# Kernel optimization log

Measured on AMD Instinct MI355X. Metric: run time of the kernel, lower is better.

## Reference

```python
import jax, jax.numpy as jnp
import numpy as np

N_MODES = 64


def setup_inputs() -> dict:
    key = jax.random.key(0)
    k1, k2, k3 = jax.random.split(key, 3)
    B, Cin, S = 32, 128, 8192
    H, Hc, M = 4, 32, N_MODES  # n_heads, head_channels, n_modes (Cout = H*Hc = 128)
    x = jax.random.normal(k1, (B, Cin, S), dtype=jnp.float32)
    # per-head init scale: std = 0.01 * 2**h (matches _init_weights)
    scale = (0.01 * 2.0 ** jnp.arange(H, dtype=jnp.float32)).reshape(H, 1, 1, 1)
    w_real = jax.random.normal(k2, (H, Cin, Hc, M), dtype=jnp.float32) * scale
    w_imag = jax.random.normal(k3, (H, Cin, Hc, M), dtype=jnp.float32) * scale
    return {"x": x, "w_real": w_real, "w_imag": w_imag}


def reference(x, w_real, w_imag):
    B, Cin, S = x.shape
    H, _, Hc, M = w_real.shape
    Cout = H * Hc
    x_ft = jnp.fft.rfft(x, axis=-1)                 # [B, Cin, F] complex64
    F = x_ft.shape[-1]
    M = min(M, F)                                    # static
    w = (w_real + 1j * w_imag).astype(x_ft.dtype)    # [H, Cin, Hc, M]
    # fused batched complex contraction over all heads/modes at once
    out = jnp.einsum('bim,hiom->bhom', x_ft[:, :, :M], w[..., :M])  # [B, H, Hc, M]
    out = out.reshape(B, Cout, M)                    # head h -> channels [h*Hc, (h+1)*Hc)
    out_ft = jnp.zeros((B, Cout, F), dtype=x_ft.dtype).at[:, :, :M].set(out)
    return jnp.fft.irfft(out_ft, n=S, axis=-1)       # [B, Cout, S] float32
```

## Files before the change

kernel.cpp:

```cpp
#include <hip/hip_runtime.h>
#include <cstdio>

#define S_LEN 8192
#define NM 64

typedef short s8v __attribute__((ext_vector_type(8)));
typedef float f4  __attribute__((ext_vector_type(4)));
typedef _Float16 h8 __attribute__((ext_vector_type(8)));

static __device__ inline unsigned short f2bf(float f) {
    unsigned int u = __builtin_bit_cast(unsigned int, f);
    u = (u + 0x7FFFu + ((u >> 16) & 1u)) >> 16;
    return (unsigned short)u;
}
static __device__ inline float bf2f(unsigned short h) {
    unsigned int u = ((unsigned int)h) << 16;
    return __builtin_bit_cast(float, u);
}

#define SW32(r, k) (((r) * 32) + ((k) ^ ((((r) >> 1) & 3) << 3)))

static __device__ __forceinline__ void glds16(const void* g, void* l) {
    __builtin_amdgcn_global_load_lds(
        (const __attribute__((address_space(1))) unsigned int*)g,
        (__attribute__((address_space(3))) unsigned int*)l, 16, 0, 0);
}

__global__ __launch_bounds__(256) void gen_master(float* __restrict__ tab) {
    int p = blockIdx.x * 256 + threadIdx.x;
    tab[p] = cosf((float)p * (6.28318530717958647692f / (float)S_LEN));
}

__global__ __launch_bounds__(256) void gen_tables(const float* __restrict__ tab,
                                                  short* __restrict__ T1fH,
                                                  short* __restrict__ T1fL,
                                                  _Float16* __restrict__ Bimg) {
    int tid = blockIdx.x * 256 + threadIdx.x;
    {
        int tile = tid >> 12;
        int sb = tile >> 2, kc = tile & 3;
        int uw = tid & 4095;
        int c = uw >> 5, rest = uw & 31;
        int k = kc * 32 + rest;
        int s = sb * 128 + c;
        int m = k >> 1;
        int p = (m * s + ((k & 1) << 11)) & (S_LEN - 1);
        float v = tab[p];
        unsigned short h = f2bf(v);
        T1fH[tid] = (short)h;
        T1fL[tid] = (short)f2bf(v - bf2f(h));
    }
    {
        int tk = tid >> 13;
        int us = tid & 8191;
        int c = us >> 6;
        int wl = us & 63;
        int slot = wl >> 3, e = wl & 7;
        int k = ((slot ^ (c & 7)) << 3) | e;
        int kg = tk * 64 + k;
        int m = c >> 1;
        int p = (m * kg + ((c & 1) << 11)) & (S_LEN - 1);
        Bimg[tid] = (_Float16)tab[p];
    }
}

__global__ __launch_bounds__(512, 4) void dft_fwd_mfma(const float* __restrict__ x,
        const _Float16* __restrict__ Bimg, float* __restrict__ P) {
    __shared__ _Float16 abh[2][4096], abl[2][4096];
    __shared__ _Float16 bb[2][8192];
    const int t = threadIdx.x;
    const int lane = t & 63, w = t >> 6;
    const int rl = lane & 15, kq = lane >> 4;
    const int wr = w >> 2, wc = w & 3;
    const int row0 = blockIdx.x * 64;
    const int ks = blockIdx.y;
    const int rA = t >> 3, sA = t & 7;
    const size_t xrow = (size_t)(row0 + rA) * S_LEN + (size_t)ks * 1024 + (size_t)sA * 8;
    const int usA = rA * 64 + ((sA ^ (rA & 7)) << 3);
    const size_t bby = (size_t)ks * 16 * 16384 + (size_t)t * 32;

    f4 acc[2][2];
    #pragma unroll
    for (int i = 0; i < 2; ++i)
        #pragma unroll
        for (int j = 0; j < 2; ++j) acc[i][j] = (f4){0.f, 0.f, 0.f, 0.f};

    f4 aP[3][2];
    h8 bP[2][2];

    #define LA_(SC, A0, A1) { A0 = *(const f4*)&x[xrow + (size_t)(SC) * 64];       \
                              A1 = *(const f4*)&x[xrow + (size_t)(SC) * 64 + 4]; }
    #define LB_(SC, B0, B1) { const char* g = (const char*)Bimg + bby +            \
                                  (size_t)(SC) * 16384;                            \
                              B0 = *(const h8*)g; B1 = *(const h8*)(g + 16); }
    #define CV_(A0, A1, NXT) { h8 hv, lv;                                          \
        _Pragma("unroll")                                                          \
        for (int e = 0; e < 4; ++e) {                                              \
            float f = A0[e]; _Float16 hh = (_Float16)f;                            \
            hv[e] = hh; lv[e] = (_Float16)(f - (float)hh);                         \
        }                                                                          \
        _Pragma("unroll")                                                          \
        for (int e = 0; e < 4; ++e) {                                              \
            float f = A1[e]; _Float16 hh = (_Float16)f;                            \
            hv[4 + e] = hh; lv[4 + e] = (_Float16)(f - (float)hh);                 \
        }                                                                          \
        *(h8*)&abh[NXT][usA] = hv;                                                 \
        *(h8*)&abl[NXT][usA] = lv; }
    #define WB_(B0, B1, NXT) { *(h8*)&bb[NXT][t * 16] = B0;                        \
                               *(h8*)&bb[NXT][t * 16 + 8] = B1; }
    #define MM_(CUR) { _Pragma("unroll")                                           \
        for (int ksl = 0; ksl < 2; ++ksl) {                                        \
            const int sb_ = ksl * 4 + kq;                                          \
            h8 Ah0, Al0, Ah1, Al1, Bv0, Bv1;                                       \
            { int r = wr * 32 + rl;      int u = r * 64 + ((sb_ ^ (r & 7)) << 3);  \
              Ah0 = *(const h8*)&abh[CUR][u]; Al0 = *(const h8*)&abl[CUR][u]; }    \
            { int r = wr * 32 + 16 + rl; int u = r * 64 + ((sb_ ^ (r & 7)) << 3);  \
              Ah1 = *(const h8*)&abh[CUR][u]; Al1 = *(const h8*)&abl[CUR][u]; }    \
            { int c = wc * 32 + rl;      int u = c * 64 + ((sb_ ^ (c & 7)) << 3);  \
              Bv0 = *(const h8*)&bb[CUR][u]; }                                     \
            { int c = wc * 32 + 16 + rl; int u = c * 64 + ((sb_ ^ (c & 7)) << 3);  \
              Bv1 = *(const h8*)&bb[CUR][u]; }                                     \
            acc[0][0] = __builtin_amdgcn_mfma_f32_16x16x32_f16(Ah0, Bv0, acc[0][0], 0, 0, 0); \
            acc[0][1] = __builtin_amdgcn_mfma_f32_16x16x32_f16(Ah0, Bv1, acc[0][1], 0, 0, 0); \
            acc[1][0] = __builtin_amdgcn_mfma_f32_16x16x32_f16(Ah1, Bv0, acc[1][0], 0, 0, 0); \
            acc[1][1] = __builtin_amdgcn_mfma_f32_16x16x32_f16(Ah1, Bv1, acc[1][1], 0, 0, 0); \
            acc[0][0] = __builtin_amdgcn_mfma_f32_16x16x32_f16(Al0, Bv0, acc[0][0], 0, 0, 0); \
            acc[0][1] = __builtin_amdgcn_mfma_f32_16x16x32_f16(Al0, Bv1, acc[0][1], 0, 0, 0); \
            acc[1][0] = __builtin_amdgcn_mfma_f32_16x16x32_f16(Al1, Bv0, acc[1][0], 0, 0, 0); \
            acc[1][1] = __builtin_amdgcn_mfma_f32_16x16x32_f16(Al1, Bv1, acc[1][1], 0, 0, 0); \
        } }
    #define BAR_ __builtin_amdgcn_sched_barrier(0);                                \
        asm volatile("s_waitcnt lgkmcnt(0)" ::: "memory");                         \
        __builtin_amdgcn_sched_barrier(0);                                         \
        __builtin_amdgcn_s_barrier();                                              \
        __builtin_amdgcn_sched_barrier(0);

    {
        f4 t0a, t0b; h8 tb0a, tb0b;
        LA_(0, t0a, t0b) LB_(0, tb0a, tb0b)
        LA_(1, aP[1][0], aP[1][1]) LA_(2, aP[2][0], aP[2][1])
        LB_(1, bP[1][0], bP[1][1])
        __builtin_amdgcn_sched_barrier(0);
        CV_(t0a, t0b, 0) WB_(tb0a, tb0b, 0)
        BAR_
    }
    #pragma unroll
    for (int s = 0; s < 16; ++s) {
        if (s + 3 <= 15) LA_(s + 3, aP[(s + 3) % 3][0], aP[(s + 3) % 3][1])
        if (s + 2 <= 15) LB_(s + 2, bP[(s + 2) & 1][0], bP[(s + 2) & 1][1])
        __builtin_amdgcn_sched_barrier(0);
        if (s + 1 <= 15) { CV_(aP[(s + 1) % 3][0], aP[(s + 1) % 3][1], (s + 1) & 1)
                           WB_(bP[(s + 1) & 1][0], bP[(s + 1) & 1][1], (s + 1) & 1) }
        MM_(s & 1)
        if (s < 15) { BAR_ }
    }

    float* Pks = P + (size_t)ks * 524288;
    #pragma unroll
    for (int mf = 0; mf < 2; ++mf)
        #pragma unroll
        for (int nf = 0; nf < 2; ++nf)
            #pragma unroll
            for (int r = 0; r < 4; ++r)
                Pks[(size_t)(row0 + wr * 32 + mf * 16 + kq * 4 + r) * 128
                    + wc * 32 + nf * 16 + rl] = acc[mf][nf][r];
}

__global__ __launch_bounds__(256) void ksum(const float* __restrict__ P,
                                            float* __restrict__ X) {
    int i = (blockIdx.x * 256 + threadIdx.x) * 4;
    f4 s = (f4){0.f, 0.f, 0.f, 0.f};
    #pragma unroll
    for (int ks = 0; ks < 8; ++ks)
        s += *(const f4*)&P[(size_t)ks * 524288 + i];
    *(f4*)&X[i] = s;
}

__global__ __launch_bounds__(256) void mode_contract(const float* __restrict__ X,
        const float* __restrict__ w_real, const float* __restrict__ w_imag,
        short* __restrict__ C2h, short* __restrict__ C2l) {
    __shared__ float xr[32][128], xi[32][128];
    __shared__ float wr[128][32], wi[128][32];
    const int m = blockIdx.x, h = blockIdx.y, t = threadIdx.x;
    #pragma unroll
    for (int it = 0; it < 16; ++it) {
        int li = t + it * 256;
        int b = li >> 7, i = li & 127;
        const float2 v = *(const float2*)&X[(size_t)(b * 128 + i) * 128 + 2 * m];
        xr[b][i] = v.x; xi[b][i] = v.y;
        int i2 = li >> 5, o = li & 31;
        size_t off = ((size_t)((h * 128 + i2) * 32 + o)) * NM + m;
        wr[i2][o] = w_real[off];
        wi[i2][o] = w_imag[off];
    }
    __syncthreads();
    const int o = t & 31;
    const int b0 = (t >> 5) * 4;
    float re[4] = {0.f, 0.f, 0.f, 0.f}, im[4] = {0.f, 0.f, 0.f, 0.f};
    for (int i = 0; i < 128; ++i) {
        float wrv = wr[i][o], wiv = wi[i][o];
        #pragma unroll
        for (int j = 0; j < 4; ++j) {
            float a = xr[b0 + j][i], c = xi[b0 + j][i];
            re[j] += a * wrv - c * wiv;
            im[j] += a * wiv + c * wrv;
        }
    }
    const float alpha = (m == 0) ? (1.0f / (float)S_LEN) : (2.0f / (float)S_LEN);
    const int kc = m >> 4;
    const int lk = (2 * m) & 31;
    #pragma unroll
    for (int j = 0; j < 4; ++j) {
        int row = (b0 + j) * 128 + h * 32 + o;
        float vr = alpha * re[j], vi = alpha * im[j];
        unsigned short hr = f2bf(vr), hi_ = f2bf(vi);
        float lr = vr - bf2f(hr), li_ = vi - bf2f(hi_);
        int rb = row >> 7, lr_ = row & 127;
        size_t ui = ((size_t)(rb * 4 + kc) * 4096 + SW32(lr_, lk)) >> 1;
        ((unsigned int*)C2h)[ui] = ((unsigned int)hi_ << 16) | hr;
        ((unsigned int*)C2l)[ui] = ((unsigned int)f2bf(li_) << 16) | f2bf(lr);
    }
}

__global__ __launch_bounds__(256, 2) void idft_mfma(const short* __restrict__ C2h,
        const short* __restrict__ C2l, const short* __restrict__ T1fH,
        const short* __restrict__ T1fL, float* __restrict__ y) {
    __shared__ short ah[4][4096], al[4][4096];
    const int t = threadIdx.x;
    const int lane = t & 63, w = t >> 6;
    const int rl = lane & 15, kq = lane >> 4;
    const int wm = (w >> 1) * 64, wn = (w & 1) * 64;
    const int sb = blockIdx.x, rb = blockIdx.y;

    #pragma unroll
    for (int kc = 0; kc < 4; ++kc) {
        const size_t ta = (size_t)(rb * 4 + kc) * 8192;
        const int wo = w * 2048 + lane * 16;
        glds16((const char*)C2h + ta + wo,        (char*)&ah[kc][0] + w * 2048);
        glds16((const char*)C2h + ta + wo + 1024, (char*)&ah[kc][0] + w * 2048 + 1024);
        glds16((const char*)C2l + ta + wo,        (char*)&al[kc][0] + w * 2048);
        glds16((const char*)C2l + ta + wo + 1024, (char*)&al[kc][0] + w * 2048 + 1024);
    }
    __syncthreads();

    f4 acc[4][4];
    #pragma unroll
    for (int i = 0; i < 4; ++i)
        #pragma unroll
        for (int j = 0; j < 4; ++j) acc[i][j] = (f4){0.f, 0.f, 0.f, 0.f};

    #pragma unroll
    for (int kc = 0; kc < 4; ++kc) {
        s8v Bh[4], Bl[4];
        const size_t tb = (size_t)(sb * 4 + kc) * 8192 + (size_t)rl * 64 + (size_t)kq * 16;
        #pragma unroll
        for (int nf = 0; nf < 4; ++nf) {
            const size_t off = tb + (size_t)(wn + nf * 16) * 64;
            Bh[nf] = *(const s8v*)((const char*)T1fH + off);
            Bl[nf] = *(const s8v*)((const char*)T1fL + off);
        }
        const int kk = kq * 8;
        s8v Ah[4], Al[4];
        #pragma unroll
        for (int mf = 0; mf < 4; ++mf) {
            int us = SW32(wm + mf * 16 + rl, kk);
            Ah[mf] = *(const s8v*)&ah[kc][us];
            Al[mf] = *(const s8v*)&al[kc][us];
        }
        #pragma unroll
        for (int mf = 0; mf < 4; ++mf)
            #pragma unroll
            for (int nf = 0; nf < 4; ++nf)
                acc[mf][nf] = __builtin_amdgcn_mfma_f32_16x16x32_bf16(Ah[mf], Bh[nf], acc[mf][nf], 0, 0, 0);
        #pragma unroll
        for (int mf = 0; mf < 4; ++mf)
            #pragma unroll
            for (int nf = 0; nf < 4; ++nf)
                acc[mf][nf] = __builtin_amdgcn_mfma_f32_16x16x32_bf16(Al[mf], Bh[nf], acc[mf][nf], 0, 0, 0);
        #pragma unroll
        for (int mf = 0; mf < 4; ++mf)
            #pragma unroll
            for (int nf = 0; nf < 4; ++nf)
                acc[mf][nf] = __builtin_amdgcn_mfma_f32_16x16x32_bf16(Ah[mf], Bl[nf], acc[mf][nf], 0, 0, 0);
    }

    #pragma unroll
    for (int mf = 0; mf < 4; ++mf) {
        int rr = rb * 128 + wm + mf * 16 + kq * 4;
        #pragma unroll
        for (int nf = 0; nf < 4; ++nf) {
            int c = sb * 128 + wn + nf * 16 + rl;
            #pragma unroll
            for (int r = 0; r < 4; ++r)
                __builtin_nontemporal_store(acc[mf][nf][r], &y[(size_t)(rr + r) * S_LEN + c]);
        }
    }
}

extern "C" void kernel_launch(void* const* d_in, const int* in_sizes, int n_in,
                              void* d_out, int out_size, void* d_ws, size_t ws_size,
                              hipStream_t stream) {
    const float* x      = (const float*)d_in[0];
    const float* w_real = (const float*)d_in[1];
    const float* w_imag = (const float*)d_in[2];
    float* y = (float*)d_out;

    const size_t TBL = (size_t)S_LEN * 128;
    char* w0 = (char*)d_ws;
    short* T1fH    = (short*)w0;
    short* T1fL    = T1fH + TBL;
    _Float16* Bimg = (_Float16*)(T1fL + TBL);
    float* X       = (float*)(Bimg + TBL);
    float* tab     = X + (size_t)4096 * 128;
    float* P       = tab + S_LEN;
    short* C2h     = (short*)P;
    short* C2l     = C2h + TBL;
    const size_t TOTAL = (size_t)((char*)(P + 8 * (size_t)4096 * 128) - w0);
    if (ws_size < TOTAL) {
        fprintf(stderr, "kernel_launch: ws too small (%zu < %zu bytes)\n", ws_size, TOTAL);
        return;
    }

    gen_master<<<S_LEN / 256, 256, 0, stream>>>(tab);
    gen_tables<<<(S_LEN * 128) / 256, 256, 0, stream>>>(tab, T1fH, T1fL, Bimg);
    dft_fwd_mfma<<<dim3(64, 8), 512, 0, stream>>>(x, Bimg, P);
    ksum<<<512, 256, 0, stream>>>(P, X);
    mode_contract<<<dim3(NM, 4), 256, 0, stream>>>(X, w_real, w_imag, C2h, C2l);
    idft_mfma<<<dim3(64, 32), 256, 0, stream>>>(C2h, C2l, T1fH, T1fL, y);
}
```

Baseline: 122.9 us.

## Transpose spectrum and weights so mode_contract loads are coalesced

The k-split reduction kernel now also transposes the summed spectrum into a mode-major layout through shared memory. A new kernel transposes the real and imaginary weights so each (head, mode) slice is contiguous. mode_contract then reads both operands with unit stride instead of gathering single floats at 256–512-byte strides. The cost is an extra launch and a full read and write of the weight tensors each call, and the reduction now runs on fewer blocks with scalar loads.

```diff
diff --git a/kernel.cpp b/kernel.cpp
--- a/kernel.cpp
+++ b/kernel.cpp
@@ -166,18 +166,58 @@
                     + wc * 32 + nf * 16 + rl] = acc[mf][nf][r];
 }
 
-__global__ __launch_bounds__(256) void ksum(const float* __restrict__ P,
-                                            float* __restrict__ X) {
-    int i = (blockIdx.x * 256 + threadIdx.x) * 4;
-    f4 s = (f4){0.f, 0.f, 0.f, 0.f};
-    #pragma unroll
-    for (int ks = 0; ks < 8; ++ks)
-        s += *(const f4*)&P[(size_t)ks * 524288 + i];
-    *(f4*)&X[i] = s;
-}
-
-__global__ __launch_bounds__(256) void mode_contract(const float* __restrict__ X,
-        const float* __restrict__ w_real, const float* __restrict__ w_imag,
+__global__ __launch_bounds__(256) void ksum_t(const float* __restrict__ P,
+                                              float* __restrict__ Xt) {
+    __shared__ float xt[32][130];
+    const int row0 = blockIdx.x * 32;
+    const int t = threadIdx.x;
+    #pragma unroll
+    for (int it = 0; it < 16; ++it) {
+        int li = t + it * 256;
+        int r = li >> 7, c = li & 127;
+        float s = 0.f;
+        #pragma unroll
+        for (int ks = 0; ks < 8; ++ks)
+            s += P[(size_t)ks * 524288 + (size_t)(row0 + r) * 128 + c];
+        xt[r][c] = s;
+    }
+    __syncthreads();
+    const int m = t >> 2, q = t & 3;
+    #pragma unroll
+    for (int j = 0; j < 8; ++j) {
+        int r = q * 8 + j;
+        float2 v = make_float2(xt[r][2 * m], xt[r][2 * m + 1]);
+        *(float2*)&Xt[((size_t)m * 4096 + row0 + r) * 2] = v;
+    }
+}
+
+__global__ __launch_bounds__(256) void wtrans(const float* __restrict__ w_real,
+                                              const float* __restrict__ w_imag,
+                                              float* __restrict__ wTr,
+                                              float* __restrict__ wTi) {
+    __shared__ float tile[64][65];
+    const int io0 = blockIdx.x * 64;
+    const int h = blockIdx.y >> 1;
+    const float* src = (blockIdx.y & 1) ? w_imag : w_real;
+    float* dst = (blockIdx.y & 1) ? wTi : wTr;
+    const int t = threadIdx.x;
+    #pragma unroll
+    for (int it = 0; it < 16; ++it) {
+        int li = t + it * 256;
+        int r = li >> 6, c = li & 63;
+        tile[r][c] = src[((size_t)h * 4096 + io0 + r) * 64 + c];
+    }
+    __syncthreads();
+    #pragma unroll
+    for (int it = 0; it < 16; ++it) {
+        int li = t + it * 256;
+        int mr = li >> 6, ioc = li & 63;
+        dst[((size_t)h * 64 + mr) * 4096 + io0 + ioc] = tile[ioc][mr];
+    }
+}
+
+__global__ __launch_bounds__(256) void mode_contract(const float* __restrict__ Xt,
+        const float* __restrict__ wTr, const float* __restrict__ wTi,
         short* __restrict__ C2h, short* __restrict__ C2l) {
     __shared__ float xr[32][128], xi[32][128];
     __shared__ float wr[128][32], wi[128][32];
@@ -185,13 +225,12 @@
     #pragma unroll
     for (int it = 0; it < 16; ++it) {
         int li = t + it * 256;
-        int b = li >> 7, i = li & 127;
-        const float2 v = *(const float2*)&X[(size_t)(b * 128 + i) * 128 + 2 * m];
-        xr[b][i] = v.x; xi[b][i] = v.y;
-        int i2 = li >> 5, o = li & 31;
-        size_t off = ((size_t)((h * 128 + i2) * 32 + o)) * NM + m;
-        wr[i2][o] = w_real[off];
-        wi[i2][o] = w_imag[off];
+        const float2 v = *(const float2*)&Xt[((size_t)m * 4096 + li) * 2];
+        xr[li >> 7][li & 127] = v.x;
+        xi[li >> 7][li & 127] = v.y;
+        const size_t woff = (size_t)(h * 64 + m) * 4096 + li;
+        wr[li >> 5][li & 31] = wTr[woff];
+        wi[li >> 5][li & 31] = wTi[woff];
     }
     __syncthreads();
     const int o = t & 31;
@@ -310,10 +349,12 @@
     short* T1fH    = (short*)w0;
     short* T1fL    = T1fH + TBL;
     _Float16* Bimg = (_Float16*)(T1fL + TBL);
-    float* X       = (float*)(Bimg + TBL);
-    float* tab     = X + (size_t)4096 * 128;
+    float* Xt      = (float*)(Bimg + TBL);
+    float* tab     = Xt + (size_t)64 * 4096 * 2;
     float* P       = tab + S_LEN;
-    short* C2h     = (short*)P;
+    float* wTr     = P;
+    float* wTi     = wTr + (size_t)4 * 64 * 4096;
+    short* C2h     = (short*)(wTi + (size_t)4 * 64 * 4096);
     short* C2l     = C2h + TBL;
     const size_t TOTAL = (size_t)((char*)(P + 8 * (size_t)4096 * 128) - w0);
     if (ws_size < TOTAL) {
@@ -324,7 +365,8 @@
     gen_master<<<S_LEN / 256, 256, 0, stream>>>(tab);
     gen_tables<<<(S_LEN * 128) / 256, 256, 0, stream>>>(tab, T1fH, T1fL, Bimg);
     dft_fwd_mfma<<<dim3(64, 8), 512, 0, stream>>>(x, Bimg, P);
-    ksum<<<512, 256, 0, stream>>>(P, X);
-    mode_contract<<<dim3(NM, 4), 256, 0, stream>>>(X, w_real, w_imag, C2h, C2l);
+    ksum_t<<<128, 256, 0, stream>>>(P, Xt);
+    wtrans<<<dim3(64, 8), 256, 0, stream>>>(w_real, w_imag, wTr, wTi);
+    mode_contract<<<dim3(NM, 4), 256, 0, stream>>>(Xt, wTr, wTi, C2h, C2l);
     idft_mfma<<<dim3(64, 32), 256, 0, stream>>>(C2h, C2l, T1fH, T1fL, y);
 }
```

Result: faster. 117.0 us (median of 4 runs) (-4.9%).
